# Kernel optimization log

Hardware: AMD Instinct MI355X
Metric: run time of the kernel (lower is better)

Reference implementation:

```python
import jax, jax.numpy as jnp
import numpy as np

B, F, R, O = 32768, 64, 64, 64  # batch, in_features, rules, out_features


def setup_inputs() -> dict:
    key = jax.random.key(0)
    k1, k2, k3, k4, k5 = jax.random.split(key, 5)
    X = jax.random.normal(k1, (B, F), dtype=jnp.float32)
    tt = jax.random.normal(k2, (1, F, R), dtype=jnp.float32) * 0.01
    mean = jax.random.normal(k3, (1, F, R), dtype=jnp.float32)
    # std is a learned positive scale (set by _rule_initialization); keep it away from 0
    std = jax.random.uniform(k4, (1, F, R), dtype=jnp.float32, minval=0.5, maxval=1.5)
    W = jax.random.normal(k5, (O, R * (F + 1)), dtype=jnp.float32) * 0.02  # nn.Linear weight [out, in]
    return {"X": X, "tt": tt, "mean": mean, "std": std, "W": W}


def reference(X, tt, mean, std, W):
    t = jnp.tanh(tt)                                  # [1,F,R]
    z = (X[:, :, None] - mean) / std                  # [B,F,R]
    g = jnp.exp(-(z * z))                             # Gaussian membership [B,F,R]
    m = g * t + 0.5 * (1.0 - t)                       # affine blend toward 0.5
    fire = jnp.prod(m, axis=1)                        # product t-norm over features -> [B,R]
    w = fire / jnp.sum(fire, axis=1, keepdims=True)   # normalize over rules
    ones = jnp.ones((X.shape[0], 1), dtype=X.dtype)
    Xa = jnp.concatenate([X, ones], axis=1)           # [B,F+1]
    feat = (Xa[:, :, None] * w[:, None, :]).reshape(X.shape[0], -1)  # [B,(F+1)*R], row-major (f outer, r inner)
    return feat @ W.T                                 # [B,O]
```

## Files before the change

kernel.cpp:

```cpp
#include <hip/hip_runtime.h>
#include <hip/hip_bf16.h>

#define F 64
#define R 64
#define O 64
#define BLOCK_B 64

typedef short bf16x8 __attribute__((ext_vector_type(8)));
typedef float f32x4 __attribute__((ext_vector_type(4)));
typedef float f32x2 __attribute__((ext_vector_type(2)));

static __device__ __forceinline__ short f2bf(float f) {
    unsigned u = __builtin_bit_cast(unsigned, f);
    unsigned r = (u + 0x7fffu + ((u >> 16) & 1u)) >> 16;
    return (short)r;
}

__global__ __launch_bounds__(256) void fq_prep(
        const float* __restrict__ tt, const float* __restrict__ mean,
        const float* __restrict__ std_, const float* __restrict__ W,
        float* __restrict__ prm, unsigned short* __restrict__ Wpk)
{
    const int tg = blockIdx.x * 256 + threadIdx.x;
    if (tg < 65 * 512) {
        const int f    = tg >> 9;
        const int u8   = tg & 511;
        const int lane = u8 & 63;
        const int kk   = (u8 >> 6) & 1;
        const int nt   = u8 >> 7;
        const int o    = nt * 16 + (lane & 15);
        const int rb   = ((lane >> 4) << 3) + kk * 32;
        const float* src = W + o * 4160 + f * 64 + rb;
        unsigned short v[8];
#pragma unroll
        for (int j = 0; j < 8; ++j) v[j] = (unsigned short)f2bf(src[j]);
        const int dst = ((nt * 65 + f) * 2 + kk) * 64 + lane;
        *(bf16x8*)(Wpk + (size_t)dst * 8) = *(bf16x8*)v;
    } else if (tg < 65 * 512 + 4096) {
        const int u = tg - 65 * 512;
        float sd = std_[u];
        float mn = mean[u];
        float th = tanhf(tt[u]);
        float s  = 1.2011224087864498f / sd;
        float4 p;
        p.x = s;
        p.y = mn * s;
        p.z = th;
        p.w = 0.5f * (1.0f - th);
        ((float4*)prm)[u] = p;
    }
}

__global__ __launch_bounds__(512, 2) void fq_main(
        const float* __restrict__ X,
        const float4* __restrict__ prm,
        const bf16x8* __restrict__ Wp,
        float* __restrict__ out)
{
    __shared__ __align__(16) float xt[64][68];
    __shared__ __align__(16) float fire_lds[64][68];
    __shared__ float rinv[BLOCK_B];

    const int t    = threadIdx.x;
    const int lane = t & 63;
    const int w    = __builtin_amdgcn_readfirstlane(t >> 6);
    const int b0   = blockIdx.x * BLOCK_B;

    const int xrow = t >> 4;
    const int xf4  = (t & 15) * 4;
    float4 xh0 = *(const float4*)(X + (size_t)(b0 + xrow) * 64 + xf4);
    float4 xh1 = *(const float4*)(X + (size_t)(b0 + xrow + 32) * 64 + xf4);

    {
        f32x2 fire2[4];
#pragma unroll
        for (int i = 0; i < 4; ++i) fire2[i] = (f32x2){1.f, 1.f};
        const float* Xw = X + (size_t)(b0 + 8 * w) * 64;
        float4 p = prm[lane];
#pragma unroll 2
        for (int f = 0; f < F; ++f) {
            const int pf = (f + 1 < 64) ? f + 1 : 63;
            float4 pn = prm[pf * 64 + lane];
            f32x2 t2 = (f32x2){p.z, p.z};
            f32x2 c2 = (f32x2){p.w, p.w};
#pragma unroll
            for (int i = 0; i < 4; ++i) {
                float x0 = Xw[(2 * i) * 64 + f];
                float x1 = Xw[(2 * i + 1) * 64 + f];
                f32x2 z;
                z.x = __builtin_fmaf(x0, p.x, -p.y);
                z.y = __builtin_fmaf(x1, p.x, -p.y);
                f32x2 nz = -(z * z);
                f32x2 g;
                g.x = __builtin_amdgcn_exp2f(nz.x);
                g.y = __builtin_amdgcn_exp2f(nz.y);
                fire2[i] *= g * t2 + c2;
            }
            p = pn;
        }
        xt[xf4 + 0][xrow] = xh0.x;  xt[xf4 + 0][xrow + 32] = xh1.x;
        xt[xf4 + 1][xrow] = xh0.y;  xt[xf4 + 1][xrow + 32] = xh1.y;
        xt[xf4 + 2][xrow] = xh0.z;  xt[xf4 + 2][xrow + 32] = xh1.z;
        xt[xf4 + 3][xrow] = xh0.w;  xt[xf4 + 3][xrow + 32] = xh1.w;
        const int r0 = 8 * w;
#pragma unroll
        for (int i = 0; i < 4; ++i) {
            fire_lds[r0 + 2 * i][lane]     = fire2[i].x;
            fire_lds[r0 + 2 * i + 1][lane] = fire2[i].y;
        }
    }
    __syncthreads();

    {
        const int row = t >> 3;
        const int c8  = (t & 7) * 8;
        f32x4 s0 = *(const f32x4*)&fire_lds[row][c8];
        f32x4 s1 = *(const f32x4*)&fire_lds[row][c8 + 4];
        float s = (s0[0] + s0[1]) + (s0[2] + s0[3]) +
                  (s1[0] + s1[1]) + (s1[2] + s1[3]);
        s += __shfl_xor(s, 1);
        s += __shfl_xor(s, 2);
        s += __shfl_xor(s, 4);
        if ((t & 7) == 0) rinv[row] = 1.0f / s;
    }
    __syncthreads();

    const int m_in = lane & 15;
    const int quad = lane >> 4;
    const int nt   = w >> 1;
    const int g    = w & 1;
    const int q8   = quad * 8;

    bf16x8 wfrag[2][2];
#pragma unroll
    for (int mm = 0; mm < 2; ++mm) {
        const int myrow = 32 * g + 16 * mm + m_in;
        const float rs  = rinv[myrow];
#pragma unroll
        for (int kk = 0; kk < 2; ++kk) {
            f32x4 a = *(const f32x4*)&fire_lds[myrow][q8 + kk * 32];
            f32x4 b = *(const f32x4*)&fire_lds[myrow][q8 + kk * 32 + 4];
            wfrag[mm][kk][0] = f2bf(a[0] * rs); wfrag[mm][kk][1] = f2bf(a[1] * rs);
            wfrag[mm][kk][2] = f2bf(a[2] * rs); wfrag[mm][kk][3] = f2bf(a[3] * rs);
            wfrag[mm][kk][4] = f2bf(b[0] * rs); wfrag[mm][kk][5] = f2bf(b[1] * rs);
            wfrag[mm][kk][6] = f2bf(b[2] * rs); wfrag[mm][kk][7] = f2bf(b[3] * rs);
        }
    }

    const bf16x8* wpb = Wp + (size_t)(nt * 130) * 64 + lane;

    f32x4 acc[2];
    acc[0] = (f32x4){0.f, 0.f, 0.f, 0.f};
    acc[1] = (f32x4){0.f, 0.f, 0.f, 0.f};
    const f32x4 z4 = (f32x4){0.f, 0.f, 0.f, 0.f};

    bf16x8 pe0 = wpb[0 * 64],  pe1 = wpb[1 * 64];
    bf16x8 po0 = wpb[2 * 64],  po1 = wpb[3 * 64];
#pragma unroll 2
    for (int i = 0; i < 32; ++i) {
        const int fe = 2 * i, fo = 2 * i + 1;
        bf16x8 ce0 = pe0, ce1 = pe1, co0 = po0, co1 = po1;
        const int se = (fe + 2 <= 64) ? fe + 2 : 64;
        const int so = (fo + 2 <= 64) ? fo + 2 : 64;
        pe0 = wpb[(2 * se) * 64];  pe1 = wpb[(2 * se + 1) * 64];
        po0 = wpb[(2 * so) * 64];  po1 = wpb[(2 * so + 1) * 64];
#pragma unroll
        for (int mm = 0; mm < 2; ++mm) {
            f32x4 U = __builtin_amdgcn_mfma_f32_16x16x32_bf16(wfrag[mm][0], ce0, z4, 0, 0, 0);
            U = __builtin_amdgcn_mfma_f32_16x16x32_bf16(wfrag[mm][1], ce1, U, 0, 0, 0);
            f32x4 xv = *(const f32x4*)&xt[fe][32 * g + 16 * mm + quad * 4];
#pragma unroll
            for (int reg = 0; reg < 4; ++reg)
                acc[mm][reg] = __builtin_fmaf(xv[reg], U[reg], acc[mm][reg]);
        }
#pragma unroll
        for (int mm = 0; mm < 2; ++mm) {
            f32x4 U = __builtin_amdgcn_mfma_f32_16x16x32_bf16(wfrag[mm][0], co0, z4, 0, 0, 0);
            U = __builtin_amdgcn_mfma_f32_16x16x32_bf16(wfrag[mm][1], co1, U, 0, 0, 0);
            f32x4 xv = *(const f32x4*)&xt[fo][32 * g + 16 * mm + quad * 4];
#pragma unroll
            for (int reg = 0; reg < 4; ++reg)
                acc[mm][reg] = __builtin_fmaf(xv[reg], U[reg], acc[mm][reg]);
        }
    }

#pragma unroll
    for (int mm = 0; mm < 2; ++mm) {
        f32x4 U = __builtin_amdgcn_mfma_f32_16x16x32_bf16(wfrag[mm][0], pe0, z4, 0, 0, 0);
        U = __builtin_amdgcn_mfma_f32_16x16x32_bf16(wfrag[mm][1], pe1, U, 0, 0, 0);
#pragma unroll
        for (int reg = 0; reg < 4; ++reg)
            acc[mm][reg] += U[reg];
    }

#pragma unroll
    for (int mm = 0; mm < 2; ++mm)
#pragma unroll
        for (int reg = 0; reg < 4; ++reg) {
            const int row = b0 + 32 * g + 16 * mm + quad * 4 + reg;
            out[(size_t)row * 64 + nt * 16 + m_in] = acc[mm][reg];
        }
}

extern "C" void kernel_launch(void* const* d_in, const int* in_sizes, int n_in,
                              void* d_out, int out_size, void* d_ws, size_t ws_size,
                              hipStream_t stream) {
    const float* X    = (const float*)d_in[0];
    const float* tt   = (const float*)d_in[1];
    const float* mean = (const float*)d_in[2];
    const float* std_ = (const float*)d_in[3];
    const float* W    = (const float*)d_in[4];
    float* out = (float*)d_out;

    float* prm = (float*)d_ws;
    unsigned short* Wpk = (unsigned short*)((char*)d_ws + 65536);

    fq_prep<<<146, 256, 0, stream>>>(tt, mean, std_, W, prm, Wpk);

    const int nblocks = 32768 / BLOCK_B;
    fq_main<<<nblocks, 512, 0, stream>>>(X, (const float4*)prm,
                                         (const bf16x8*)Wpk, out);
}
```

Before: 108.0 us.

## Double threads per block and split GEMM feature loop across wave halves

Raises the block size from 512 to 1024 threads, so each wave computes firing strengths for 4 rows instead of 8. The per-feature MFMA loop is split between two wave halves, and the partial accumulators are combined through a new shared-memory epilogue buffer. The goal is more parallelism and latency hiding per sample block, at the cost of an extra barrier and LDS traffic, and with launch bounds (1024,4) that may constrain registers.

```diff
diff --git a/kernel.cpp b/kernel.cpp
--- a/kernel.cpp
+++ b/kernel.cpp
@@ -51,7 +51,7 @@
     }
 }
 
-__global__ __launch_bounds__(512, 2) void fq_main(
+__global__ __launch_bounds__(1024, 4) void fq_main(
         const float* __restrict__ X,
         const float4* __restrict__ prm,
         const bf16x8* __restrict__ Wp,
@@ -60,6 +60,7 @@
     __shared__ __align__(16) float xt[64][68];
     __shared__ __align__(16) float fire_lds[64][68];
     __shared__ float rinv[BLOCK_B];
+    __shared__ __align__(16) float epi[16][64][4];
 
     const int t    = threadIdx.x;
     const int lane = t & 63;
@@ -68,14 +69,11 @@
 
     const int xrow = t >> 4;
     const int xf4  = (t & 15) * 4;
-    float4 xh0 = *(const float4*)(X + (size_t)(b0 + xrow) * 64 + xf4);
-    float4 xh1 = *(const float4*)(X + (size_t)(b0 + xrow + 32) * 64 + xf4);
+    float4 xh = *(const float4*)(X + (size_t)(b0 + xrow) * 64 + xf4);
 
     {
-        f32x2 fire2[4];
-#pragma unroll
-        for (int i = 0; i < 4; ++i) fire2[i] = (f32x2){1.f, 1.f};
-        const float* Xw = X + (size_t)(b0 + 8 * w) * 64;
+        f32x2 fire2[2] = {(f32x2){1.f, 1.f}, (f32x2){1.f, 1.f}};
+        const float* Xw = X + (size_t)(b0 + 4 * w) * 64;
         float4 p = prm[lane];
 #pragma unroll 2
         for (int f = 0; f < F; ++f) {
@@ -84,51 +82,50 @@
             f32x2 t2 = (f32x2){p.z, p.z};
             f32x2 c2 = (f32x2){p.w, p.w};
 #pragma unroll
-            for (int i = 0; i < 4; ++i) {
+            for (int i = 0; i < 2; ++i) {
                 float x0 = Xw[(2 * i) * 64 + f];
                 float x1 = Xw[(2 * i + 1) * 64 + f];
                 f32x2 z;
                 z.x = __builtin_fmaf(x0, p.x, -p.y);
                 z.y = __builtin_fmaf(x1, p.x, -p.y);
                 f32x2 nz = -(z * z);
-                f32x2 g;
-                g.x = __builtin_amdgcn_exp2f(nz.x);
-                g.y = __builtin_amdgcn_exp2f(nz.y);
-                fire2[i] *= g * t2 + c2;
+                f32x2 g2;
+                g2.x = __builtin_amdgcn_exp2f(nz.x);
+                g2.y = __builtin_amdgcn_exp2f(nz.y);
+                fire2[i] *= g2 * t2 + c2;
             }
             p = pn;
         }
-        xt[xf4 + 0][xrow] = xh0.x;  xt[xf4 + 0][xrow + 32] = xh1.x;
-        xt[xf4 + 1][xrow] = xh0.y;  xt[xf4 + 1][xrow + 32] = xh1.y;
-        xt[xf4 + 2][xrow] = xh0.z;  xt[xf4 + 2][xrow + 32] = xh1.z;
-        xt[xf4 + 3][xrow] = xh0.w;  xt[xf4 + 3][xrow + 32] = xh1.w;
-        const int r0 = 8 * w;
-#pragma unroll
-        for (int i = 0; i < 4; ++i) {
-            fire_lds[r0 + 2 * i][lane]     = fire2[i].x;
-            fire_lds[r0 + 2 * i + 1][lane] = fire2[i].y;
-        }
+        xt[xf4 + 0][xrow] = xh.x;
+        xt[xf4 + 1][xrow] = xh.y;
+        xt[xf4 + 2][xrow] = xh.z;
+        xt[xf4 + 3][xrow] = xh.w;
+        const int r0 = 4 * w;
+        fire_lds[r0 + 0][lane] = fire2[0].x;
+        fire_lds[r0 + 1][lane] = fire2[0].y;
+        fire_lds[r0 + 2][lane] = fire2[1].x;
+        fire_lds[r0 + 3][lane] = fire2[1].y;
     }
     __syncthreads();
 
     {
-        const int row = t >> 3;
-        const int c8  = (t & 7) * 8;
-        f32x4 s0 = *(const f32x4*)&fire_lds[row][c8];
-        f32x4 s1 = *(const f32x4*)&fire_lds[row][c8 + 4];
-        float s = (s0[0] + s0[1]) + (s0[2] + s0[3]) +
-                  (s1[0] + s1[1]) + (s1[2] + s1[3]);
+        const int row = t >> 4;
+        const int c4  = (t & 15) * 4;
+        f32x4 s4 = *(const f32x4*)&fire_lds[row][c4];
+        float s = (s4[0] + s4[1]) + (s4[2] + s4[3]);
         s += __shfl_xor(s, 1);
         s += __shfl_xor(s, 2);
         s += __shfl_xor(s, 4);
-        if ((t & 7) == 0) rinv[row] = 1.0f / s;
+        s += __shfl_xor(s, 8);
+        if ((t & 15) == 0) rinv[row] = 1.0f / s;
     }
     __syncthreads();
 
     const int m_in = lane & 15;
     const int quad = lane >> 4;
-    const int nt   = w >> 1;
-    const int g    = w & 1;
+    const int nt   = w >> 2;
+    const int g    = (w >> 1) & 1;
+    const int fh   = w & 1;
     const int q8   = quad * 8;
 
     bf16x8 wfrag[2][2];
@@ -148,58 +145,59 @@
     }
 
     const bf16x8* wpb = Wp + (size_t)(nt * 130) * 64 + lane;
+    const int f0 = fh * 32;
 
     f32x4 acc[2];
     acc[0] = (f32x4){0.f, 0.f, 0.f, 0.f};
     acc[1] = (f32x4){0.f, 0.f, 0.f, 0.f};
     const f32x4 z4 = (f32x4){0.f, 0.f, 0.f, 0.f};
 
-    bf16x8 pe0 = wpb[0 * 64],  pe1 = wpb[1 * 64];
-    bf16x8 po0 = wpb[2 * 64],  po1 = wpb[3 * 64];
+    bf16x8 p0 = wpb[(2 * f0) * 64];
+    bf16x8 p1 = wpb[(2 * f0 + 1) * 64];
 #pragma unroll 2
     for (int i = 0; i < 32; ++i) {
-        const int fe = 2 * i, fo = 2 * i + 1;
-        bf16x8 ce0 = pe0, ce1 = pe1, co0 = po0, co1 = po1;
-        const int se = (fe + 2 <= 64) ? fe + 2 : 64;
-        const int so = (fo + 2 <= 64) ? fo + 2 : 64;
-        pe0 = wpb[(2 * se) * 64];  pe1 = wpb[(2 * se + 1) * 64];
-        po0 = wpb[(2 * so) * 64];  po1 = wpb[(2 * so + 1) * 64];
+        const int f = f0 + i;
+        bf16x8 c0 = p0, c1 = p1;
+        const int sp = (f + 1 < 64) ? f + 1 : 64;
+        p0 = wpb[(2 * sp) * 64];
+        p1 = wpb[(2 * sp + 1) * 64];
 #pragma unroll
         for (int mm = 0; mm < 2; ++mm) {
-            f32x4 U = __builtin_amdgcn_mfma_f32_16x16x32_bf16(wfrag[mm][0], ce0, z4, 0, 0, 0);
-            U = __builtin_amdgcn_mfma_f32_16x16x32_bf16(wfrag[mm][1], ce1, U, 0, 0, 0);
-            f32x4 xv = *(const f32x4*)&xt[fe][32 * g + 16 * mm + quad * 4];
+            f32x4 U = __builtin_amdgcn_mfma_f32_16x16x32_bf16(wfrag[mm][0], c0, z4, 0, 0, 0);
+            U = __builtin_amdgcn_mfma_f32_16x16x32_bf16(wfrag[mm][1], c1, U, 0, 0, 0);
+            f32x4 xv = *(const f32x4*)&xt[f][32 * g + 16 * mm + quad * 4];
 #pragma unroll
             for (int reg = 0; reg < 4; ++reg)
                 acc[mm][reg] = __builtin_fmaf(xv[reg], U[reg], acc[mm][reg]);
         }
+    }
+
+    if (fh == 1) {
 #pragma unroll
         for (int mm = 0; mm < 2; ++mm) {
-            f32x4 U = __builtin_amdgcn_mfma_f32_16x16x32_bf16(wfrag[mm][0], co0, z4, 0, 0, 0);
-            U = __builtin_amdgcn_mfma_f32_16x16x32_bf16(wfrag[mm][1], co1, U, 0, 0, 0);
-            f32x4 xv = *(const f32x4*)&xt[fo][32 * g + 16 * mm + quad * 4];
+            f32x4 U = __builtin_amdgcn_mfma_f32_16x16x32_bf16(wfrag[mm][0], p0, z4, 0, 0, 0);
+            U = __builtin_amdgcn_mfma_f32_16x16x32_bf16(wfrag[mm][1], p1, U, 0, 0, 0);
 #pragma unroll
             for (int reg = 0; reg < 4; ++reg)
-                acc[mm][reg] = __builtin_fmaf(xv[reg], U[reg], acc[mm][reg]);
-        }
-    }
-
-#pragma unroll
-    for (int mm = 0; mm < 2; ++mm) {
-        f32x4 U = __builtin_amdgcn_mfma_f32_16x16x32_bf16(wfrag[mm][0], pe0, z4, 0, 0, 0);
-        U = __builtin_amdgcn_mfma_f32_16x16x32_bf16(wfrag[mm][1], pe1, U, 0, 0, 0);
-#pragma unroll
-        for (int reg = 0; reg < 4; ++reg)
-            acc[mm][reg] += U[reg];
-    }
-
-#pragma unroll
-    for (int mm = 0; mm < 2; ++mm)
-#pragma unroll
-        for (int reg = 0; reg < 4; ++reg) {
-            const int row = b0 + 32 * g + 16 * mm + quad * 4 + reg;
-            out[(size_t)row * 64 + nt * 16 + m_in] = acc[mm][reg];
-        }
+                acc[mm][reg] += U[reg];
+        }
+#pragma unroll
+        for (int mm = 0; mm < 2; ++mm)
+            *(f32x4*)&epi[(nt * 2 + g) * 2 + mm][lane][0] = acc[mm];
+    }
+    __syncthreads();
+
+    if (fh == 0) {
+#pragma unroll
+        for (int mm = 0; mm < 2; ++mm) {
+            f32x4 r = acc[mm] + *(const f32x4*)&epi[(nt * 2 + g) * 2 + mm][lane][0];
+#pragma unroll
+            for (int reg = 0; reg < 4; ++reg) {
+                const int row = b0 + 32 * g + 16 * mm + quad * 4 + reg;
+                out[(size_t)row * 64 + nt * 16 + m_in] = r[reg];
+            }
+        }
+    }
 }
 
 extern "C" void kernel_launch(void* const* d_in, const int* in_sizes, int n_in,
@@ -218,6 +216,6 @@
     fq_prep<<<146, 256, 0, stream>>>(tt, mean, std_, W, prm, Wpk);
 
     const int nblocks = 32768 / BLOCK_B;
-    fq_main<<<nblocks, 512, 0, stream>>>(X, (const float4*)prm,
-                                         (const bf16x8*)Wpk, out);
-}
+    fq_main<<<nblocks, 1024, 0, stream>>>(X, (const float4*)prm,
+                                          (const bf16x8*)Wpk, out);
+}
```

After: 108.7 us. Within noise of the previous version (+0.7%).

## Defer rule normalization to output, store fire as bf16, hoist W prefetch

Applied to the files above, without the earlier changes.

Unnormalized firing strengths are now converted to bf16 and written straight to LDS, which removes one barrier and the separate row-sum pass. The row sums are computed with wavefront shuffle reductions, and the reciprocal is applied to the final accumulators, since the output is linear in w. The first W fragment loads are issued before the Gaussian loop to hide their latency. The risk is a precision change: unnormalized fire values may be very small and lose bf16 dynamic range or underflow before the scaling is applied.

```diff
diff --git a/kernel.cpp b/kernel.cpp
--- a/kernel.cpp
+++ b/kernel.cpp
@@ -10,10 +10,10 @@
 typedef float f32x4 __attribute__((ext_vector_type(4)));
 typedef float f32x2 __attribute__((ext_vector_type(2)));
 
-static __device__ __forceinline__ short f2bf(float f) {
+static __device__ __forceinline__ unsigned short f2bf(float f) {
     unsigned u = __builtin_bit_cast(unsigned, f);
     unsigned r = (u + 0x7fffu + ((u >> 16) & 1u)) >> 16;
-    return (short)r;
+    return (unsigned short)r;
 }
 
 __global__ __launch_bounds__(256) void fq_prep(
@@ -33,7 +33,7 @@
         const float* src = W + o * 4160 + f * 64 + rb;
         unsigned short v[8];
 #pragma unroll
-        for (int j = 0; j < 8; ++j) v[j] = (unsigned short)f2bf(src[j]);
+        for (int j = 0; j < 8; ++j) v[j] = f2bf(src[j]);
         const int dst = ((nt * 65 + f) * 2 + kk) * 64 + lane;
         *(bf16x8*)(Wpk + (size_t)dst * 8) = *(bf16x8*)v;
     } else if (tg < 65 * 512 + 4096) {
@@ -58,18 +58,24 @@
         float* __restrict__ out)
 {
     __shared__ __align__(16) float xt[64][68];
-    __shared__ __align__(16) float fire_lds[64][68];
-    __shared__ float rinv[BLOCK_B];
+    __shared__ __align__(16) unsigned short fireb[64][72];
+    __shared__ __align__(16) float rinv[BLOCK_B];
 
     const int t    = threadIdx.x;
     const int lane = t & 63;
     const int w    = __builtin_amdgcn_readfirstlane(t >> 6);
     const int b0   = blockIdx.x * BLOCK_B;
+    const int nt   = w >> 1;
+    const int g    = w & 1;
 
     const int xrow = t >> 4;
     const int xf4  = (t & 15) * 4;
     float4 xh0 = *(const float4*)(X + (size_t)(b0 + xrow) * 64 + xf4);
     float4 xh1 = *(const float4*)(X + (size_t)(b0 + xrow + 32) * 64 + xf4);
+
+    const bf16x8* wpb = Wp + (size_t)(nt * 130) * 64 + lane;
+    bf16x8 pe0 = wpb[0 * 64],  pe1 = wpb[1 * 64];
+    bf16x8 po0 = wpb[2 * 64],  po1 = wpb[3 * 64];
 
     {
         f32x2 fire2[4];
@@ -91,10 +97,10 @@
                 z.x = __builtin_fmaf(x0, p.x, -p.y);
                 z.y = __builtin_fmaf(x1, p.x, -p.y);
                 f32x2 nz = -(z * z);
-                f32x2 g;
-                g.x = __builtin_amdgcn_exp2f(nz.x);
-                g.y = __builtin_amdgcn_exp2f(nz.y);
-                fire2[i] *= g * t2 + c2;
+                f32x2 g2;
+                g2.x = __builtin_amdgcn_exp2f(nz.x);
+                g2.y = __builtin_amdgcn_exp2f(nz.y);
+                fire2[i] *= g2 * t2 + c2;
             }
             p = pn;
         }
@@ -105,57 +111,42 @@
         const int r0 = 8 * w;
 #pragma unroll
         for (int i = 0; i < 4; ++i) {
-            fire_lds[r0 + 2 * i][lane]     = fire2[i].x;
-            fire_lds[r0 + 2 * i + 1][lane] = fire2[i].y;
-        }
-    }
-    __syncthreads();
-
-    {
-        const int row = t >> 3;
-        const int c8  = (t & 7) * 8;
-        f32x4 s0 = *(const f32x4*)&fire_lds[row][c8];
-        f32x4 s1 = *(const f32x4*)&fire_lds[row][c8 + 4];
-        float s = (s0[0] + s0[1]) + (s0[2] + s0[3]) +
-                  (s1[0] + s1[1]) + (s1[2] + s1[3]);
-        s += __shfl_xor(s, 1);
-        s += __shfl_xor(s, 2);
-        s += __shfl_xor(s, 4);
-        if ((t & 7) == 0) rinv[row] = 1.0f / s;
+            fireb[r0 + 2 * i][lane]     = f2bf(fire2[i].x);
+            fireb[r0 + 2 * i + 1][lane] = f2bf(fire2[i].y);
+        }
+#pragma unroll
+        for (int i = 0; i < 4; ++i) {
+            float sx = fire2[i].x, sy = fire2[i].y;
+#pragma unroll
+            for (int d = 1; d < 64; d <<= 1) {
+                sx += __shfl_xor(sx, d);
+                sy += __shfl_xor(sy, d);
+            }
+            if (lane == 0) {
+                rinv[r0 + 2 * i]     = 1.0f / sx;
+                rinv[r0 + 2 * i + 1] = 1.0f / sy;
+            }
+        }
     }
     __syncthreads();
 
     const int m_in = lane & 15;
     const int quad = lane >> 4;
-    const int nt   = w >> 1;
-    const int g    = w & 1;
-    const int q8   = quad * 8;
+    const int q16  = quad * 16;
 
     bf16x8 wfrag[2][2];
 #pragma unroll
     for (int mm = 0; mm < 2; ++mm) {
         const int myrow = 32 * g + 16 * mm + m_in;
-        const float rs  = rinv[myrow];
-#pragma unroll
-        for (int kk = 0; kk < 2; ++kk) {
-            f32x4 a = *(const f32x4*)&fire_lds[myrow][q8 + kk * 32];
-            f32x4 b = *(const f32x4*)&fire_lds[myrow][q8 + kk * 32 + 4];
-            wfrag[mm][kk][0] = f2bf(a[0] * rs); wfrag[mm][kk][1] = f2bf(a[1] * rs);
-            wfrag[mm][kk][2] = f2bf(a[2] * rs); wfrag[mm][kk][3] = f2bf(a[3] * rs);
-            wfrag[mm][kk][4] = f2bf(b[0] * rs); wfrag[mm][kk][5] = f2bf(b[1] * rs);
-            wfrag[mm][kk][6] = f2bf(b[2] * rs); wfrag[mm][kk][7] = f2bf(b[3] * rs);
-        }
-    }
-
-    const bf16x8* wpb = Wp + (size_t)(nt * 130) * 64 + lane;
+        wfrag[mm][0] = *(const bf16x8*)((const char*)&fireb[myrow][0] + q16);
+        wfrag[mm][1] = *(const bf16x8*)((const char*)&fireb[myrow][32] + q16);
+    }
 
     f32x4 acc[2];
     acc[0] = (f32x4){0.f, 0.f, 0.f, 0.f};
     acc[1] = (f32x4){0.f, 0.f, 0.f, 0.f};
     const f32x4 z4 = (f32x4){0.f, 0.f, 0.f, 0.f};
 
-    bf16x8 pe0 = wpb[0 * 64],  pe1 = wpb[1 * 64];
-    bf16x8 po0 = wpb[2 * 64],  po1 = wpb[3 * 64];
 #pragma unroll 2
     for (int i = 0; i < 32; ++i) {
         const int fe = 2 * i, fo = 2 * i + 1;
@@ -194,12 +185,14 @@
     }
 
 #pragma unroll
-    for (int mm = 0; mm < 2; ++mm)
+    for (int mm = 0; mm < 2; ++mm) {
+        f32x4 rv = *(const f32x4*)&rinv[32 * g + 16 * mm + quad * 4];
 #pragma unroll
         for (int reg = 0; reg < 4; ++reg) {
             const int row = b0 + 32 * g + 16 * mm + quad * 4 + reg;
-            out[(size_t)row * 64 + nt * 16 + m_in] = acc[mm][reg];
-        }
+            out[(size_t)row * 64 + nt * 16 + m_in] = acc[mm][reg] * rv[reg];
+        }
+    }
 }
 
 extern "C" void kernel_launch(void* const* d_in, const int* in_sizes, int n_in,
```

Measured after the change: 103.1 us. 4.5% less time.
